# Kernel tuning notes

Measured on AMD Instinct MI355X. Metric: run time of the kernel, lower is better.

The kernel has to match this reference:

```python
import jax, jax.numpy as jnp
import numpy as np

HIDDEN = 1024
HEADS = 16
HEAD_DIM = HIDDEN // HEADS
BATCH = 1
SEQ = 4096
SCALE = 1.0 / np.sqrt(HEAD_DIM)


def setup_inputs() -> dict:
    key = jax.random.key(0)
    ks = jax.random.split(key, 5)
    s = 0.02
    return {
        "hidden_states": jax.random.normal(ks[0], (BATCH, SEQ, HIDDEN), jnp.float32),
        "qkv_w": jax.random.normal(ks[1], (3 * HIDDEN, HIDDEN), jnp.float32) * s,
        "qkv_b": jax.random.normal(ks[2], (3 * HIDDEN,), jnp.float32) * s,
        "out_w": jax.random.normal(ks[3], (HIDDEN, HIDDEN), jnp.float32) * s,
        "out_b": jax.random.normal(ks[4], (HIDDEN,), jnp.float32) * s,
    }


def reference(hidden_states, qkv_w, qkv_b, out_w, out_b):
    B, S, H = hidden_states.shape
    # fused QKV projection (torch Linear: x @ W^T + b)
    qkv = hidden_states @ qkv_w.T + qkv_b              # [B, S, 3H]
    qkv = qkv.reshape(B, S, 3, HEADS, HEAD_DIM)
    qkv = jnp.transpose(qkv, (2, 0, 3, 1, 4))          # [3, B, nh, S, hd]
    q, k, v = qkv[0] * SCALE, qkv[1], qkv[2]
    # ring attention over all KV chunks == full softmax attention
    scores = jnp.einsum('bhqd,bhkd->bhqk', q, k)       # [B, nh, S, S]
    probs = jax.nn.softmax(scores, axis=-1)
    ctx = jnp.einsum('bhqk,bhkd->bhqd', probs, v)      # [B, nh, S, hd]
    ctx = jnp.transpose(ctx, (0, 2, 1, 3)).reshape(B, S, H)
    return ctx @ out_w.T + out_b
```

## Files before the change

### kernel.cpp

```cpp
#include <hip/hip_runtime.h>

#define SEQ 4096
#define HID 1024
#define NHEADS 16
#define HDIM 64
#define QK_SCALE 0.1803368801111204f

typedef float  f32x4 __attribute__((ext_vector_type(4)));
typedef int    i32x4 __attribute__((ext_vector_type(4)));
typedef int    i32x2 __attribute__((ext_vector_type(2)));
typedef __bf16 bf16x8 __attribute__((ext_vector_type(8)));
typedef unsigned short u16;
typedef unsigned int   u32;

static __device__ __forceinline__ u16 f2bf(float f) {
  u32 u = __builtin_bit_cast(u32, f);
  return (u16)((u + 0x7FFFu + ((u >> 16) & 1u)) >> 16);
}
static __device__ __forceinline__ int cvtpk(float lo, float hi) {
  int r;
  asm("v_cvt_pk_bf16_f32 %0, %1, %2" : "=v"(r) : "v"(lo), "v"(hi));
  return r;
}
static __device__ __forceinline__ f32x4 exp2v(f32x4 x) {
  f32x4 o;
  o.x = __builtin_amdgcn_exp2f(x.x);
  o.y = __builtin_amdgcn_exp2f(x.y);
  o.z = __builtin_amdgcn_exp2f(x.z);
  o.w = __builtin_amdgcn_exp2f(x.w);
  return o;
}
static __device__ __forceinline__ float sum4(f32x4 x) {
  return (x.x + x.y) + (x.z + x.w);
}
static __device__ __forceinline__ f32x4 mfma16(i32x4 a, i32x4 b, f32x4 c) {
  return __builtin_amdgcn_mfma_f32_16x16x32_bf16(
      __builtin_bit_cast(bf16x8, a), __builtin_bit_cast(bf16x8, b), c, 0, 0, 0);
}

#define GLD(gsrc, lds_dst)                                        \
  __builtin_amdgcn_global_load_lds(                               \
      (const __attribute__((address_space(1))) void*)(gsrc),      \
      (__attribute__((address_space(3))) void*)(lds_dst), 16, 0, 0)

__global__ __launch_bounds__(256) void cvt_kernel(
    const float* __restrict__ X, const float* __restrict__ Wq,
    const float* __restrict__ Wo, u16* __restrict__ Xb,
    u16* __restrict__ Wqb, u16* __restrict__ Wob) {
  const int u = blockIdx.x * 256 + threadIdx.x;
  const float* src; u16* dst; int local;
  if (u < 524288)       { src = X;  dst = Xb;  local = u; }
  else if (u < 917504)  { src = Wq; dst = Wqb; local = u - 524288; }
  else                  { src = Wo; dst = Wob; local = u - 917504; }
  const int row = local >> 7, gu = local & 127;
  const int w = gu & 7, blk = gu >> 3;
  const int ks = w >> 2, q2 = w & 3;
  const float* s = src + (size_t)row * 1024 + blk * 64 + ks * 32 + q2 * 4;
  float4 x0 = *(const float4*)s;
  float4 x1 = *(const float4*)(s + 16);
  i32x4 o = {cvtpk(x0.x, x0.y), cvtpk(x0.z, x0.w),
             cvtpk(x1.x, x1.y), cvtpk(x1.z, x1.w)};
  *(i32x4*)(dst + (size_t)row * 1024 + blk * 64 + w * 8) = o;
}

static __device__ __forceinline__ void gemm_tile(
    const u16* __restrict__ A, const u16* __restrict__ B,
    int mb, int nb, u16 (*LA)[128][64], u16 (*LB)[128][64],
    f32x4 acc[4][4]) {
  const int t = threadIdx.x, lane = t & 63, wv = t >> 6;
  const int g = lane >> 4, r = lane & 15;
  const int wr = wv >> 1, wc = wv & 1;
  const int lr = lane >> 3, sl = lane & 7;

  const u16* pa = A + (size_t)(mb + wv * 32 + lr) * 1024 + ((sl ^ lr) << 3);
  const u16* pb = B + (size_t)(nb + wv * 32 + lr) * 1024 + ((sl ^ lr) << 3);

  const u16* afp[4][2];
  const u16* bfp[4][2];
#pragma unroll
  for (int i = 0; i < 4; ++i)
#pragma unroll
    for (int ks = 0; ks < 2; ++ks) {
      const int sw = r & 7;
      afp[i][ks] = &LA[0][wr * 64 + i * 16 + r][(((ks * 4 + g) ^ sw) << 3)];
      bfp[i][ks] = &LB[0][wc * 64 + i * 16 + r][(((ks * 4 + g) ^ sw) << 3)];
    }
#pragma unroll
  for (int i = 0; i < 4; ++i)
#pragma unroll
    for (int j = 0; j < 4; ++j) acc[i][j] = (f32x4)0.0f;

#pragma unroll
  for (int j = 0; j < 4; ++j) {
    GLD(pa + j * 8 * 1024, &LA[0][wv * 32 + j * 8][0]);
    GLD(pb + j * 8 * 1024, &LB[0][wv * 32 + j * 8][0]);
  }
  pa += 64; pb += 64;
  __syncthreads();

#define GEMM_STEP(BU, PRE)                                                  \
  {                                                                         \
    if (PRE) {                                                              \
      _Pragma("unroll")                                                     \
      for (int j = 0; j < 4; ++j) {                                         \
        GLD(pa + j * 8 * 1024, &LA[(BU) ^ 1][wv * 32 + j * 8][0]);          \
        GLD(pb + j * 8 * 1024, &LB[(BU) ^ 1][wv * 32 + j * 8][0]);          \
      }                                                                     \
      pa += 64; pb += 64;                                                   \
    }                                                                       \
    i32x4 af[4][2], bf[4][2];                                               \
    _Pragma("unroll")                                                       \
    for (int i = 0; i < 4; ++i)                                             \
      _Pragma("unroll")                                                     \
      for (int ks = 0; ks < 2; ++ks) {                                      \
        af[i][ks] = *(const i32x4*)(afp[i][ks] + (BU) * 8192);              \
        bf[i][ks] = *(const i32x4*)(bfp[i][ks] + (BU) * 8192);              \
      }                                                                     \
    __builtin_amdgcn_s_setprio(1);                                          \
    _Pragma("unroll")                                                       \
    for (int ks = 0; ks < 2; ++ks)                                          \
      _Pragma("unroll")                                                     \
      for (int i = 0; i < 4; ++i)                                           \
        _Pragma("unroll")                                                   \
        for (int j = 0; j < 4; ++j)                                         \
          acc[i][j] = mfma16(af[i][ks], bf[j][ks], acc[i][j]);              \
    __builtin_amdgcn_s_setprio(0);                                          \
    __syncthreads();                                                        \
  }

  for (int kk = 0; kk < 8; ++kk) {
    GEMM_STEP(0, true)
    GEMM_STEP(1, (kk < 7))
  }
#undef GEMM_STEP
}

__global__ __launch_bounds__(256) void qkv_kernel(
    const u16* __restrict__ A, const u16* __restrict__ Bw,
    const float* __restrict__ BI, u16* __restrict__ qws,
    u16* __restrict__ kws, u16* __restrict__ vws) {
  __shared__ u16 LA[2][128][64];
  __shared__ u16 LB[2][128][64];
  const int t = threadIdx.x, lane = t & 63, wv = t >> 6;
  const int g = lane >> 4, r = lane & 15;
  const int wr = wv >> 1, wc = wv & 1;
  const int mb = blockIdx.x * 128, nb = blockIdx.y * 128;

  f32x4 acc[4][4];
  gemm_tile(A, Bw, mb, nb, LA, LB, acc);

#pragma unroll
  for (int ni = 0; ni < 4; ni++) {
    const int n = nb + wc * 64 + ni * 16 + r;
    const float bias = BI[n];
    const int which = n >> 10;
    const int h = (n >> 6) & 15;
    const int d = n & 63;
    u16* dst = (which == 0) ? qws : (which == 1) ? kws : vws;
    const float sc = (which == 0) ? QK_SCALE : 1.0f;
    const int dq = (which == 2)
        ? d
        : ((d & 32) | (((d >> 2) & 3) << 3) | (((d >> 4) & 1) << 2) | (d & 3));
#pragma unroll
    for (int mi = 0; mi < 4; mi++) {
      const int m0 = mb + wr * 64 + mi * 16 + g * 4;
#pragma unroll
      for (int e = 0; e < 4; e += 2) {
        float v0 = (acc[mi][ni][e] + bias) * sc;
        float v1 = (acc[mi][ni][e + 1] + bias) * sc;
        int w = cvtpk(v0, v1);
        dst[((size_t)h * SEQ + m0 + e) * HDIM + dq] = (u16)w;
        dst[((size_t)h * SEQ + m0 + e + 1) * HDIM + dq] = (u16)(w >> 16);
      }
    }
  }
}

__global__ __launch_bounds__(256, 2) void attn_kernel(
    const u16* __restrict__ qws, const u16* __restrict__ kws,
    const u16* __restrict__ vws, u16* __restrict__ ctx) {
  __shared__ u16 Kl[2][64][64];
  __shared__ u16 Vl[2][16][256];
  const int t = threadIdx.x;
  const int lane = t & 63, wv = t >> 6;
  const int g = lane >> 4, r = lane & 15;

  const int fb = blockIdx.x;
  const int swz = (fb & 7) * 64 + (fb >> 3);
  const int h = swz >> 5;
  const int qb = (swz & 31) * 128 + wv * 32;

  i32x4 qf[2][2];
#pragma unroll
  for (int qt = 0; qt < 2; qt++)
#pragma unroll
    for (int db = 0; db < 2; db++)
      qf[qt][db] = *(const i32x4*)(qws +
          ((size_t)(h * SEQ + qb + qt * 16 + r) * HDIM + db * 32 + g * 8));

  f32x4 acc[2][4];
  f32x4 l4[2];
  const f32x4 zero4 = (f32x4)0.0f;
#pragma unroll
  for (int qt = 0; qt < 2; qt++) {
    l4[qt] = (f32x4)0.0f;
#pragma unroll
    for (int dc = 0; dc < 4; dc++) acc[qt][dc] = (f32x4)0.0f;
  }

  const u16* kh_base = kws + (size_t)h * SEQ * HDIM;
  const u16* vh_base = vws + (size_t)h * SEQ * HDIM;

  const u16* kgA = kh_base + (size_t)(16 * wv + (lane >> 3)) * HDIM +
                   (((lane & 7) ^ ((lane >> 3) & 7)) << 3);
  const u16* kgB = kgA + 8 * HDIM;
  const u16* vgA = vh_base +
                   (size_t)(wv * 16 + ((lane & 31) >> 1)) * HDIM +
                   (((((lane >> 5) << 1) | (lane & 1))) << 3);
  const u16* vgB = vgA + 32;

  const u16* kfp0[4];
  const u16* kfp1[4];
#pragma unroll
  for (int kt = 0; kt < 4; ++kt) {
    const int R = kt * 16 + r;
    const int sw = R & 7;
    kfp0[kt] = &Kl[0][R][(g ^ sw) << 3];
    kfp1[kt] = &Kl[0][R][((4 + g) ^ sw) << 3];
  }
  const u32 vbase = (u32)(size_t)(&Vl[0][0][0]) + (u32)lane * 8;

  GLD(kgA, &Kl[0][wv * 16][0]);
  GLD(kgB, &Kl[0][wv * 16 + 8][0]);
  GLD(vgA, &Vl[0][wv * 4][0]);
  GLD(vgB, &Vl[0][wv * 4 + 2][0]);
  kgA += 4096; kgB += 4096; vgA += 4096; vgB += 4096;
  __syncthreads();

#define TRG(a0, a1, a2, a3, addr)                                           \
  asm volatile(                                                             \
      "ds_read_b64_tr_b16 %0, %4 offset:0\n\t"                              \
      "ds_read_b64_tr_b16 %1, %4 offset:2048\n\t"                           \
      "ds_read_b64_tr_b16 %2, %4 offset:4096\n\t"                           \
      "ds_read_b64_tr_b16 %3, %4 offset:6144"                               \
      : "=&v"(a0), "=&v"(a1), "=&v"(a2), "=&v"(a3)                          \
      : "v"(addr))
#define LGKM(N)                                                             \
  asm volatile("s_waitcnt lgkmcnt(" #N ")" ::: "memory");                   \
  __builtin_amdgcn_sched_barrier(0)
#define PVMFMA(dc, a0, a1, a2, a3)                                          \
  {                                                                         \
    i32x4 vf0 = {a0.x, a0.y, a1.x, a1.y};                                   \
    i32x4 vf1 = {a2.x, a2.y, a3.x, a3.y};                                   \
    acc[0][dc] = mfma16(pf[0][0], vf0, acc[0][dc]);                         \
    acc[0][dc] = mfma16(pf[0][1], vf1, acc[0][dc]);                         \
    acc[1][dc] = mfma16(pf[1][0], vf0, acc[1][dc]);                         \
    acc[1][dc] = mfma16(pf[1][1], vf1, acc[1][dc]);                         \
  }

#define ATTN_STEP(B, PRE)                                                   \
  {                                                                         \
    if (PRE) {                                                              \
      GLD(kgA, &Kl[(B) ^ 1][wv * 16][0]);                                   \
      GLD(kgB, &Kl[(B) ^ 1][wv * 16 + 8][0]);                               \
      GLD(vgA, &Vl[(B) ^ 1][wv * 4][0]);                                    \
      GLD(vgB, &Vl[(B) ^ 1][wv * 4 + 2][0]);                                \
      kgA += 4096; kgB += 4096; vgA += 4096; vgB += 4096;                   \
    }                                                                       \
    f32x4 st[2][4];                                                         \
    __builtin_amdgcn_s_setprio(1);                                          \
    _Pragma("unroll")                                                       \
    for (int kt = 0; kt < 4; ++kt) {                                        \
      i32x4 kf0 = *(const i32x4*)(kfp0[kt] + (B) * 4096);                   \
      i32x4 kf1 = *(const i32x4*)(kfp1[kt] + (B) * 4096);                   \
      st[0][kt] = mfma16(kf0, qf[0][0], zero4);                             \
      st[0][kt] = mfma16(kf1, qf[0][1], st[0][kt]);                         \
      st[1][kt] = mfma16(kf0, qf[1][0], zero4);                             \
      st[1][kt] = mfma16(kf1, qf[1][1], st[1][kt]);                         \
    }                                                                       \
    __builtin_amdgcn_s_setprio(0);                                          \
    const u32 vb = vbase + (B) * 8192;                                      \
    i32x2 t00, t01, t02, t03, t10, t11, t12, t13;                           \
    i32x2 t20, t21, t22, t23, t30, t31, t32, t33;                           \
                   \
    TRG(t00, t01, t02, t03, vb);                                            \
    TRG(t10, t11, t12, t13, vb + 512);                                      \
                          \
    i32x4 pf[2][2];                                                         \
    _Pragma("unroll")                                                       \
    for (int qt = 0; qt < 2; ++qt) {                                        \
      f32x4 p0 = exp2v(st[qt][0]);                                          \
      f32x4 p1 = exp2v(st[qt][1]);                                          \
      f32x4 p2 = exp2v(st[qt][2]);                                          \
      f32x4 p3 = exp2v(st[qt][3]);                                          \
      l4[qt] += p0; l4[qt] += p1; l4[qt] += p2; l4[qt] += p3;               \
      pf[qt][0] = (i32x4){cvtpk(p0.x, p0.y), cvtpk(p0.z, p0.w),             \
                          cvtpk(p1.x, p1.y), cvtpk(p1.z, p1.w)};            \
      pf[qt][1] = (i32x4){cvtpk(p2.x, p2.y), cvtpk(p2.z, p2.w),             \
                          cvtpk(p3.x, p3.y), cvtpk(p3.z, p3.w)};            \
    }                                                                       \
                       \
    TRG(t20, t21, t22, t23, vb + 1024);                                     \
    __builtin_amdgcn_s_setprio(1);                                          \
    LGKM(8);                                                   \
    PVMFMA(0, t00, t01, t02, t03)                                           \
    TRG(t30, t31, t32, t33, vb + 1536);                                     \
    LGKM(8);                                                   \
    PVMFMA(1, t10, t11, t12, t13)                                           \
    LGKM(4);                                                   \
    PVMFMA(2, t20, t21, t22, t23)                                           \
    LGKM(0);                                                   \
    PVMFMA(3, t30, t31, t32, t33)                                           \
    __builtin_amdgcn_s_setprio(0);                                          \
    __syncthreads();                                                        \
  }

  for (int cc = 0; cc < 32; ++cc) {
    ATTN_STEP(0, true)
    ATTN_STEP(1, (cc < 31))
  }
#undef ATTN_STEP
#undef TRG
#undef LGKM
#undef PVMFMA

#pragma unroll
  for (int qt = 0; qt < 2; ++qt) {
    float lsum = sum4(l4[qt]);
    lsum += __shfl_xor(lsum, 16);
    lsum += __shfl_xor(lsum, 32);
#pragma unroll
    for (int rr = 0; rr < 4; ++rr) {
      const float lr_ = __shfl(lsum, 4 * g + rr);
      const float inv = 1.0f / lr_;
      const int s_ = qb + qt * 16 + 4 * g + rr;
#pragma unroll
      for (int dc = 0; dc < 4; ++dc) {
        const int shuf = ((dc >> 1) << 5) | ((r >> 2) << 3) | ((dc & 1) << 2) | (r & 3);
        ctx[(size_t)s_ * HID + h * HDIM + shuf] = f2bf(acc[qt][dc][rr] * inv);
      }
    }
  }
}

__global__ __launch_bounds__(256) void out_kernel(
    const u16* __restrict__ A, const u16* __restrict__ Bw,
    const float* __restrict__ BI, float* __restrict__ out) {
  __shared__ u16 LA[2][128][64];
  __shared__ u16 LB[2][128][64];
  const int t = threadIdx.x, lane = t & 63, wv = t >> 6;
  const int g = lane >> 4, r = lane & 15;
  const int wr = wv >> 1, wc = wv & 1;
  const int mb = blockIdx.x * 128, nb = blockIdx.y * 128;

  f32x4 acc[4][4];
  gemm_tile(A, Bw, mb, nb, LA, LB, acc);

#pragma unroll
  for (int ni = 0; ni < 4; ni++) {
    const int n = nb + wc * 64 + ni * 16 + r;
    const float bias = BI[n];
#pragma unroll
    for (int mi = 0; mi < 4; mi++) {
      const int m0 = mb + wr * 64 + mi * 16 + g * 4;
#pragma unroll
      for (int e = 0; e < 4; e++)
        out[(size_t)(m0 + e) * HID + n] = acc[mi][ni][e] + bias;
    }
  }
}

extern "C" void kernel_launch(void* const* d_in, const int* in_sizes, int n_in,
                              void* d_out, int out_size, void* d_ws, size_t ws_size,
                              hipStream_t stream) {
  const float* X    = (const float*)d_in[0];
  const float* Wqkv = (const float*)d_in[1];
  const float* Bqkv = (const float*)d_in[2];
  const float* Wout = (const float*)d_in[3];
  const float* Bout = (const float*)d_in[4];
  float* out = (float*)d_out;

  const size_t per = (size_t)NHEADS * SEQ * HDIM;
  u16* qws = (u16*)d_ws;
  u16* kws = qws + per;
  u16* vws = kws + per;
  u16* xbctx = vws + per;
  u16* wqb = xbctx + per;
  u16* wob = wqb + (size_t)3072 * 1024;

  cvt_kernel<<<4096, 256, 0, stream>>>(X, Wqkv, Wout, xbctx, wqb, wob);
  qkv_kernel<<<dim3(32, 24), 256, 0, stream>>>(xbctx, wqb, Bqkv, qws, kws, vws);
  attn_kernel<<<dim3(512), 256, 0, stream>>>(qws, kws, vws, xbctx);
  out_kernel<<<dim3(32, 8), 256, 0, stream>>>(xbctx, wob, Bout, out);
}
```

Measured before the change: 138.5 us.

## Split attention KV range in halves and add a combine kernel

```diff
diff --git a/kernel.cpp b/kernel.cpp
--- a/kernel.cpp
+++ b/kernel.cpp
@@ -11,11 +11,15 @@
 typedef int    i32x2 __attribute__((ext_vector_type(2)));
 typedef __bf16 bf16x8 __attribute__((ext_vector_type(8)));
 typedef unsigned short u16;
+typedef unsigned short u16x4 __attribute__((ext_vector_type(4)));
 typedef unsigned int   u32;
 
 static __device__ __forceinline__ u16 f2bf(float f) {
   u32 u = __builtin_bit_cast(u32, f);
   return (u16)((u + 0x7FFFu + ((u >> 16) & 1u)) >> 16);
+}
+static __device__ __forceinline__ float bf2f(u16 v) {
+  return __builtin_bit_cast(float, (u32)v << 16);
 }
 static __device__ __forceinline__ int cvtpk(float lo, float hi) {
   int r;
@@ -176,9 +180,10 @@
   }
 }
 
-__global__ __launch_bounds__(256, 2) void attn_kernel(
+__global__ __launch_bounds__(256, 4) void attn_kernel(
     const u16* __restrict__ qws, const u16* __restrict__ kws,
-    const u16* __restrict__ vws, u16* __restrict__ ctx) {
+    const u16* __restrict__ vws, u16* __restrict__ Ab,
+    float* __restrict__ lb) {
   __shared__ u16 Kl[2][64][64];
   __shared__ u16 Vl[2][16][256];
   const int t = threadIdx.x;
@@ -186,8 +191,10 @@
   const int g = lane >> 4, r = lane & 15;
 
   const int fb = blockIdx.x;
-  const int swz = (fb & 7) * 64 + (fb >> 3);
-  const int h = swz >> 5;
+  const int swz = (fb & 7) * 128 + (fb >> 3);
+  const int hg = swz >> 5;
+  const int h = hg >> 1;
+  const int half = hg & 1;
   const int qb = (swz & 31) * 128 + wv * 32;
 
   i32x4 qf[2][2];
@@ -208,8 +215,8 @@
     for (int dc = 0; dc < 4; dc++) acc[qt][dc] = (f32x4)0.0f;
   }
 
-  const u16* kh_base = kws + (size_t)h * SEQ * HDIM;
-  const u16* vh_base = vws + (size_t)h * SEQ * HDIM;
+  const u16* kh_base = kws + (size_t)(h * SEQ + half * 2048) * HDIM;
+  const u16* vh_base = vws + (size_t)(h * SEQ + half * 2048) * HDIM;
 
   const u16* kgA = kh_base + (size_t)(16 * wv + (lane >> 3)) * HDIM +
                    (((lane & 7) ^ ((lane >> 3) & 7)) << 3);
@@ -315,9 +322,9 @@
     __syncthreads();                                                        \
   }
 
-  for (int cc = 0; cc < 32; ++cc) {
+  for (int cc = 0; cc < 16; ++cc) {
     ATTN_STEP(0, true)
-    ATTN_STEP(1, (cc < 31))
+    ATTN_STEP(1, (cc < 15))
   }
 #undef ATTN_STEP
 #undef TRG
@@ -329,18 +336,39 @@
     float lsum = sum4(l4[qt]);
     lsum += __shfl_xor(lsum, 16);
     lsum += __shfl_xor(lsum, 32);
+    if (lane < 16)
+      lb[(size_t)half * 65536 + (h << 12) + qb + qt * 16 + lane] = lsum;
 #pragma unroll
     for (int rr = 0; rr < 4; ++rr) {
-      const float lr_ = __shfl(lsum, 4 * g + rr);
-      const float inv = 1.0f / lr_;
       const int s_ = qb + qt * 16 + 4 * g + rr;
-#pragma unroll
-      for (int dc = 0; dc < 4; ++dc) {
-        const int shuf = ((dc >> 1) << 5) | ((r >> 2) << 3) | ((dc & 1) << 2) | (r & 3);
-        ctx[(size_t)s_ * HID + h * HDIM + shuf] = f2bf(acc[qt][dc][rr] * inv);
-      }
+      u16* arow = Ab + (size_t)half * (NHEADS * SEQ * HDIM) +
+                  (((size_t)(h << 12) + s_) << 6);
+#pragma unroll
+      for (int dc = 0; dc < 4; ++dc)
+        arow[dc * 16 + r] = f2bf(acc[qt][dc][rr]);
     }
   }
+}
+
+__global__ __launch_bounds__(256) void combine_kernel(
+    const u16* __restrict__ Ab, const float* __restrict__ lb,
+    u16* __restrict__ ctx) {
+  const int u = blockIdx.x * 256 + threadIdx.x;
+  const int row16 = u >> 4, tq = u & 15;
+  const int h = row16 >> 12, srow = row16 & 4095;
+  const int d0 = tq << 2;
+  const size_t per = (size_t)NHEADS * SEQ * HDIM;
+  u16x4 a0 = *(const u16x4*)(Ab + ((size_t)row16 << 6) + d0);
+  u16x4 a1 = *(const u16x4*)(Ab + per + ((size_t)row16 << 6) + d0);
+  const float inv = 1.0f / (lb[row16] + lb[65536 + row16]);
+  float o0 = (bf2f(a0.x) + bf2f(a1.x)) * inv;
+  float o1 = (bf2f(a0.y) + bf2f(a1.y)) * inv;
+  float o2 = (bf2f(a0.z) + bf2f(a1.z)) * inv;
+  float o3 = (bf2f(a0.w) + bf2f(a1.w)) * inv;
+  const int dc = d0 >> 4;
+  const int shufb = ((dc >> 1) << 5) | (((d0 >> 2) & 3) << 3) | ((dc & 1) << 2);
+  i32x2 w = {cvtpk(o0, o1), cvtpk(o2, o3)};
+  *(i32x2*)(ctx + (size_t)srow * 1024 + h * 64 + shufb) = w;
 }
 
 __global__ __launch_bounds__(256) void out_kernel(
@@ -387,9 +415,12 @@
   u16* xbctx = vws + per;
   u16* wqb = xbctx + per;
   u16* wob = wqb + (size_t)3072 * 1024;
+  u16* Ab  = wob + (size_t)1024 * 1024;
+  float* lbuf = (float*)(Ab + 2 * per);
 
   cvt_kernel<<<4096, 256, 0, stream>>>(X, Wqkv, Wout, xbctx, wqb, wob);
   qkv_kernel<<<dim3(32, 24), 256, 0, stream>>>(xbctx, wqb, Bqkv, qws, kws, vws);
-  attn_kernel<<<dim3(512), 256, 0, stream>>>(qws, kws, vws, xbctx);
+  attn_kernel<<<dim3(1024), 256, 0, stream>>>(qws, kws, vws, Ab, lbuf);
+  combine_kernel<<<4096, 256, 0, stream>>>(Ab, lbuf, xbctx);
   out_kernel<<<dim3(32, 8), 256, 0, stream>>>(xbctx, wob, Bout, out);
 }
```

New measurement: 142.5 us. 1.03x slower.
